# Performance work log

Hardware: AMD Instinct MI355X
Metric: run time of the kernel (lower is better)

Reference implementation:

```python
import jax, jax.numpy as jnp
import numpy as np
from jax import lax

R = 3                      # blob_r
S = 2 * R + 1              # 7: maxpool / neighborhood kernel size
THRESH = 0.997
PS_XY = 0.1                # vs_xy
PS_Z = 0.02                # vs_z
ZMIN = -2.0                # zrange[0]
K_PEAKS = 131072           # static upper bound replacing torch.nonzero

_offs = np.arange(S)
_gz, _gy, _gx = np.meshgrid(_offs, _offs, _offs, indexing='ij')  # patch axis order [z,y,x]
GZ = jnp.asarray(_gz.ravel(), dtype=jnp.int32)
GY = jnp.asarray(_gy.ravel(), dtype=jnp.int32)
GX = jnp.asarray(_gx.ravel(), dtype=jnp.int32)
# centroid filters: offsets -r..r along the matching patch axis (matches torch meshgrid layout)
FZ = jnp.asarray((_gz.ravel() - R).astype(np.float32))
FY = jnp.asarray((_gy.ravel() - R).astype(np.float32))
FX = jnp.asarray((_gx.ravel() - R).astype(np.float32))


def setup_inputs() -> dict:
    key = jax.random.key(0)
    pred_vol = jax.random.uniform(key, (1, 1, 128, 512, 512), dtype=jnp.float32)
    return {"pred_vol": pred_vol, "max_peaks": K_PEAKS}


def _forward(pred_vol, max_peaks):
    vol = pred_vol[0, 0]                               # [D,H,W]
    D, H, W = vol.shape
    thr = jnp.where(vol > THRESH, vol, 0.0)
    # MaxPool3d(kernel=2r+1, stride=1, padding=r) == SAME max window (pad with -inf)
    mp = lax.reduce_window(thr, -jnp.inf, lax.max, (S, S, S), (1, 1, 1), [(R, R)] * 3)
    conf = jnp.where((mp > 0.0) & (mp == thr), mp, 0.0)  # local maxima above threshold
    # fixed-size peak extraction (replaces torch.nonzero); zero-valued entries are padding
    vals, idx = lax.top_k(conf.reshape(-1), max_peaks)   # [K], [K]
    z = idx // (H * W)
    y = (idx % (H * W)) // W
    x = idx % W
    padv = jnp.pad(vol, R)                               # ConstantPad3d(r, 0)
    # gather (2r+1)^3 neighborhoods around each peak: [K, S^3]
    patches = padv[z[:, None] + GZ[None, :], y[:, None] + GY[None, :], x[:, None] + GX[None, :]]
    s0 = patches.sum(axis=1)                             # conv3d with ones filter == conf_rec sum
    xloc = jnp.einsum('kp,p->k', patches, FX) / s0
    yloc = jnp.einsum('kp,p->k', patches, FY) / s0
    zloc = jnp.einsum('kp,p->k', patches, FZ) / s0
    xf = x.astype(jnp.float32)
    yf = y.astype(jnp.float32)
    zf = z.astype(jnp.float32)
    xrec = (xf + xloc - (W - 1) / 2.0) * PS_XY
    yrec = (yf + yloc - (H - 1) / 2.0) * PS_XY
    zrec = (zf + zloc + 0.5) * PS_Z + ZMIN
    valid = vals > 0.0
    xyz = jnp.where(valid[:, None], jnp.stack((xrec, yrec, zrec), axis=1), 0.0)  # [K,3]
    out = jnp.concatenate([xyz, vals[:, None]], axis=1)  # [K,4] = (x,y,z,conf), padded rows are 0
    return out, valid


def reference(pred_vol, max_peaks):
    return _forward(pred_vol, max_peaks)
```

## Files before the change

kernel.cpp:

```cpp
#include <hip/hip_runtime.h>

#define DD 128
#define HH 512
#define WW 512
#define NVOX (DD*HH*WW)
#define THRESHV 0.997f
#define KPEAKS 131072
#define PEAK_CAP (1u<<18)
#define NBINS 65536


__global__ void k_init(unsigned* counters, unsigned* hist, unsigned long long* sorted) {
    unsigned t = blockIdx.x * 256u + threadIdx.x;
    if (t < 64) counters[t] = 0u;
    if (t < NBINS) hist[t] = 0u;
    if (t < PEAK_CAP) sorted[t] = 0ull;
}

__global__ void k_find(const float4* __restrict__ vol4, const float* __restrict__ vol,
                       unsigned* counters, unsigned* hist,
                       unsigned long long* keys, float4* psums) {
    __shared__ unsigned lcnt, pcnt, lbase;
    __shared__ unsigned cidx[512];
    __shared__ unsigned long long lbuf[256];
    __shared__ float4 sbuf[256];
    if (threadIdx.x == 0) { lcnt = 0; pcnt = 0; }
    __syncthreads();

    unsigned base4 = blockIdx.x * 2048u + threadIdx.x;
    float4 v[8];
#pragma unroll
    for (int i = 0; i < 8; i++) v[i] = vol4[base4 + i * 256u];
    unsigned m = 0u;
#pragma unroll
    for (int i = 0; i < 8; i++) {
        m |= (v[i].x > THRESHV ? 1u : 0u) << (4 * i);
        m |= (v[i].y > THRESHV ? 1u : 0u) << (4 * i + 1);
        m |= (v[i].z > THRESHV ? 1u : 0u) << (4 * i + 2);
        m |= (v[i].w > THRESHV ? 1u : 0u) << (4 * i + 3);
    }
    while (m) {
        int b = __ffs(m) - 1;
        m &= m - 1u;
        unsigned f4 = base4 + (unsigned)(b >> 2) * 256u;
        cidx[atomicAdd(&lcnt, 1u) & 511u] = f4 * 4u + (unsigned)(b & 3);
    }
    __syncthreads();

    unsigned n = lcnt > 512u ? 512u : lcnt;
    int lane = threadIdx.x & 63;
    int wv = threadIdx.x >> 6;
    int dz = lane / 7, dy = lane - dz * 7;
    for (unsigned ci = (unsigned)wv; ci < n; ci += 4u) {
        unsigned idx = cidx[ci];
        int z = idx >> 18, y = (idx >> 9) & 511, x = idx & 511;
        float center = vol[idx];
        int nz = z + dz - 3, ny = y + dy - 3;
        bool rowok = (lane < 49) && ((unsigned)nz < DD) && ((unsigned)ny < HH);
        size_t rowbase = rowok ? (((size_t)(unsigned)nz << 18) | ((size_t)(unsigned)ny << 9))
                               : (((size_t)z << 18) | ((size_t)y << 9));
        float rv[7];
        if (x >= 3 && x <= WW - 4) {
            float4 f0 = *(const float4*)(vol + rowbase + (unsigned)(x - 3));
            float4 f1 = *(const float4*)(vol + rowbase + (unsigned)(x + 1));
            rv[0] = f0.x; rv[1] = f0.y; rv[2] = f0.z; rv[3] = f0.w;
            rv[4] = f1.x; rv[5] = f1.y; rv[6] = f1.z;
        } else {
#pragma unroll
            for (int d = 0; d < 7; d++) {
                int nx = x + d - 3;
                bool ok = (unsigned)nx < WW;
                float vv = vol[rowbase + (unsigned)(ok ? nx : x)];
                rv[d] = ok ? vv : 0.f;
            }
        }
        if (!rowok) {
#pragma unroll
            for (int d = 0; d < 7; d++) rv[d] = 0.f;
        }
        bool kill = false;
        float s0r = 0.f, sxr = 0.f;
#pragma unroll
        for (int d = 0; d < 7; d++) {
            kill |= rv[d] > center;
            s0r += rv[d];
            sxr += rv[d] * (float)(d - 3);
        }
        if (!__any(kill)) {
            float s0 = s0r, sx = sxr;
            float sy = s0r * (float)(dy - 3);
            float sz = s0r * (float)(dz - 3);
            for (int off = 32; off; off >>= 1) {
                s0 += __shfl_down(s0, off);
                sx += __shfl_down(sx, off);
                sy += __shfl_down(sy, off);
                sz += __shfl_down(sz, off);
            }
            if (lane == 0) {
                unsigned bits = __float_as_uint(center);
                atomicAdd(&hist[(~bits) & 0xFFFFu], 1u);
                unsigned li = atomicAdd(&pcnt, 1u);
                if (li < 256u) {
                    lbuf[li] = ((unsigned long long)bits << 32) | idx;
                    sbuf[li] = make_float4(s0, sx, sy, sz);
                }
            }
        }
    }
    __syncthreads();
    if (threadIdx.x == 0) lbase = atomicAdd(&counters[1], pcnt);
    __syncthreads();
    unsigned np = pcnt > 256u ? 256u : pcnt;
    for (unsigned i = threadIdx.x; i < np; i += 256u) {
        unsigned p = lbase + i;
        if (p < PEAK_CAP) { keys[p] = lbuf[i]; psums[p] = sbuf[i]; }
    }
}

__global__ void k_scan(const unsigned* __restrict__ hist, unsigned* cursor) {
    __shared__ unsigned partial[1024];
    int t = threadIdx.x;
    const uint4* h4 = (const uint4*)(hist + t * 64);
    uint4 loc[16];
#pragma unroll
    for (int i = 0; i < 16; i++) loc[i] = h4[i];
    unsigned s = 0;
#pragma unroll
    for (int i = 0; i < 16; i++) s += loc[i].x + loc[i].y + loc[i].z + loc[i].w;
    partial[t] = s;
    __syncthreads();
    for (int off = 1; off < 1024; off <<= 1) {
        unsigned v = (t >= off) ? partial[t - off] : 0u;
        __syncthreads();
        partial[t] += v;
        __syncthreads();
    }
    unsigned run = (t == 0) ? 0u : partial[t - 1];
    uint4* c4 = (uint4*)(cursor + t * 64);
#pragma unroll
    for (int i = 0; i < 16; i++) {
        uint4 h = loc[i]; uint4 o;
        o.x = run; run += h.x;
        o.y = run; run += h.y;
        o.z = run; run += h.z;
        o.w = run; run += h.w;
        c4[i] = o;
    }
}

__global__ void k_scatter(const unsigned* __restrict__ counters,
                          const unsigned long long* __restrict__ keys,
                          unsigned* cursor, unsigned long long* sorted,
                          unsigned* sslot) {
    unsigned np = counters[1]; if (np > PEAK_CAP) np = PEAK_CAP;
    unsigned t = blockIdx.x * 256u + threadIdx.x;
    if (t < np) {
        unsigned long long key = keys[t];
        unsigned bits = (unsigned)(key >> 32);
        unsigned pos = atomicAdd(&cursor[(~bits) & 0xFFFFu], 1u);
        if (pos < PEAK_CAP) { sorted[pos] = key; sslot[pos] = t; }
    }
}

__global__ void k_tiefix(const unsigned long long* __restrict__ sorted,
                         const unsigned* __restrict__ sslot,
                         unsigned long long* outk, unsigned* oslot) {
    unsigned t = blockIdx.x * 256u + threadIdx.x;
    if (t >= PEAK_CAP) return;
    unsigned long long key = sorted[t];
    unsigned bits = (unsigned)(key >> 32);
    if (bits == 0u) { outk[t] = 0ull; return; }
    unsigned s = t;
    while (s > 0 && (unsigned)(sorted[s - 1] >> 32) == bits) s--;
    unsigned myidx = (unsigned)key;
    unsigned rank = 0, e = s;
    while (e < PEAK_CAP) {
        unsigned long long k2 = sorted[e];
        if ((unsigned)(k2 >> 32) != bits) break;
        if ((unsigned)k2 < myidx) rank++;
        e++;
    }
    outk[s + rank] = key;
    oslot[s + rank] = sslot[t];
}

__global__ void k_out(const unsigned long long* __restrict__ outk,
                      const unsigned* __restrict__ oslot,
                      const float4* __restrict__ psums,
                      float4* __restrict__ out, float* __restrict__ valid) {
    unsigned row = blockIdx.x * 256u + threadIdx.x;
    if (row >= KPEAKS) return;
    unsigned long long key = outk[row];
    unsigned bits = (unsigned)(key >> 32);
    if (bits == 0u) {
        out[row] = make_float4(0.f, 0.f, 0.f, 0.f);
        valid[row] = 0.f;
        return;
    }
    unsigned idx = (unsigned)key;
    int z = idx >> 18, y = (idx >> 9) & 511, x = idx & 511;
    float4 s = psums[oslot[row]];
    float val = __uint_as_float(bits);
    float xloc = s.y / s.x, yloc = s.z / s.x, zloc = s.w / s.x;
    float xr = ((float)x + xloc - (float)(WW - 1) * 0.5f) * 0.1f;
    float yr = ((float)y + yloc - (float)(HH - 1) * 0.5f) * 0.1f;
    float zr = ((float)z + zloc + 0.5f) * 0.02f - 2.0f;
    out[row] = make_float4(xr, yr, zr, val);
    valid[row] = 1.f;
}

extern "C" void kernel_launch(void* const* d_in, const int* in_sizes, int n_in,
                              void* d_out, int out_size, void* d_ws, size_t ws_size,
                              hipStream_t stream) {
    const float* vol = (const float*)d_in[0];

    char* w = (char*)d_ws;
    unsigned* counters = (unsigned*)w;
    unsigned* hist     = (unsigned*)(w + 1024);
    unsigned* cursor   = (unsigned*)(w + 1024 + NBINS * 4);
    char* w2 = w + 1024 + 2 * NBINS * 4;
    unsigned long long* keys   = (unsigned long long*)w2;
    unsigned long long* sorted = keys + PEAK_CAP;
    unsigned long long* keyout = sorted + PEAK_CAP;
    unsigned* sslot = (unsigned*)(keyout + PEAK_CAP);
    unsigned* oslot = sslot + PEAK_CAP;
    float4*   psums = (float4*)(oslot + PEAK_CAP);

    float* out_rows = (float*)d_out;
    float* valid = out_rows + (size_t)KPEAKS * 4;

    k_init<<<PEAK_CAP / 256, 256, 0, stream>>>(counters, hist, sorted);
    k_find<<<NVOX / 8192, 256, 0, stream>>>((const float4*)vol, vol, counters, hist, keys, psums);
    k_scan<<<1, 1024, 0, stream>>>(hist, cursor);
    k_scatter<<<PEAK_CAP / 256, 256, 0, stream>>>(counters, keys, cursor, sorted, sslot);
    k_tiefix<<<PEAK_CAP / 256, 256, 0, stream>>>(sorted, sslot, keyout, oslot);
    k_out<<<(KPEAKS + 255) / 256, 256, 0, stream>>>(keyout, oslot, psums, (float4*)out_rows, valid);
}
```

Baseline: 261.2 us.

## Process two candidates per wave and fuse tie-fix with output kernel

The candidate-verification loop now handles two candidate voxels per wavefront iteration, issuing both sets of neighborhood loads together, and takes the center value from a lane shuffle instead of a separate global load. The tie-fix kernel now writes final output rows directly, which removes the intermediate key/slot arrays and the separate output kernel. Zero-filling of padding rows moves into the scatter kernel for rows at or beyond the peak count. The aim is more memory-level parallelism in the find kernel and one fewer launch plus less intermediate traffic, at the cost of higher register use and wasted work when a candidate pair is unbalanced.

Result: no change. 261.7 us (+0.2%).

```diff
diff --git a/kernel.cpp b/kernel.cpp
--- a/kernel.cpp
+++ b/kernel.cpp
@@ -51,58 +51,112 @@
     int lane = threadIdx.x & 63;
     int wv = threadIdx.x >> 6;
     int dz = lane / 7, dy = lane - dz * 7;
-    for (unsigned ci = (unsigned)wv; ci < n; ci += 4u) {
-        unsigned idx = cidx[ci];
-        int z = idx >> 18, y = (idx >> 9) & 511, x = idx & 511;
-        float center = vol[idx];
-        int nz = z + dz - 3, ny = y + dy - 3;
-        bool rowok = (lane < 49) && ((unsigned)nz < DD) && ((unsigned)ny < HH);
-        size_t rowbase = rowok ? (((size_t)(unsigned)nz << 18) | ((size_t)(unsigned)ny << 9))
-                               : (((size_t)z << 18) | ((size_t)y << 9));
-        float rv[7];
-        if (x >= 3 && x <= WW - 4) {
-            float4 f0 = *(const float4*)(vol + rowbase + (unsigned)(x - 3));
-            float4 f1 = *(const float4*)(vol + rowbase + (unsigned)(x + 1));
-            rv[0] = f0.x; rv[1] = f0.y; rv[2] = f0.z; rv[3] = f0.w;
-            rv[4] = f1.x; rv[5] = f1.y; rv[6] = f1.z;
+    for (unsigned base = (unsigned)wv * 2u; base < n; base += 8u) {
+        bool has2 = (base + 1u < n);
+        unsigned idxA = cidx[base];
+        unsigned idxB = has2 ? cidx[base + 1u] : idxA;
+        int zA = idxA >> 18, yA = (idxA >> 9) & 511, xA = idxA & 511;
+        int zB = idxB >> 18, yB = (idxB >> 9) & 511, xB = idxB & 511;
+        int nzA = zA + dz - 3, nyA = yA + dy - 3;
+        int nzB = zB + dz - 3, nyB = yB + dy - 3;
+        bool rowokA = (lane < 49) && ((unsigned)nzA < DD) && ((unsigned)nyA < HH);
+        bool rowokB = (lane < 49) && ((unsigned)nzB < DD) && ((unsigned)nyB < HH);
+        size_t rbA = rowokA ? (((size_t)(unsigned)nzA << 18) | ((size_t)(unsigned)nyA << 9))
+                            : (((size_t)zA << 18) | ((size_t)yA << 9));
+        size_t rbB = rowokB ? (((size_t)(unsigned)nzB << 18) | ((size_t)(unsigned)nyB << 9))
+                            : (((size_t)zB << 18) | ((size_t)yB << 9));
+        float rvA[7], rvB[7];
+        bool intAB = (xA >= 3) && (xA <= WW - 4) && (xB >= 3) && (xB <= WW - 4);
+        if (intAB) {
+            float4 fA0 = *(const float4*)(vol + rbA + (unsigned)(xA - 3));
+            float4 fA1 = *(const float4*)(vol + rbA + (unsigned)(xA + 1));
+            float4 fB0 = *(const float4*)(vol + rbB + (unsigned)(xB - 3));
+            float4 fB1 = *(const float4*)(vol + rbB + (unsigned)(xB + 1));
+            rvA[0] = fA0.x; rvA[1] = fA0.y; rvA[2] = fA0.z; rvA[3] = fA0.w;
+            rvA[4] = fA1.x; rvA[5] = fA1.y; rvA[6] = fA1.z;
+            rvB[0] = fB0.x; rvB[1] = fB0.y; rvB[2] = fB0.z; rvB[3] = fB0.w;
+            rvB[4] = fB1.x; rvB[5] = fB1.y; rvB[6] = fB1.z;
         } else {
 #pragma unroll
             for (int d = 0; d < 7; d++) {
-                int nx = x + d - 3;
-                bool ok = (unsigned)nx < WW;
-                float vv = vol[rowbase + (unsigned)(ok ? nx : x)];
-                rv[d] = ok ? vv : 0.f;
-            }
-        }
-        if (!rowok) {
-#pragma unroll
-            for (int d = 0; d < 7; d++) rv[d] = 0.f;
-        }
-        bool kill = false;
-        float s0r = 0.f, sxr = 0.f;
-#pragma unroll
-        for (int d = 0; d < 7; d++) {
-            kill |= rv[d] > center;
-            s0r += rv[d];
-            sxr += rv[d] * (float)(d - 3);
-        }
-        if (!__any(kill)) {
-            float s0 = s0r, sx = sxr;
-            float sy = s0r * (float)(dy - 3);
-            float sz = s0r * (float)(dz - 3);
-            for (int off = 32; off; off >>= 1) {
-                s0 += __shfl_down(s0, off);
-                sx += __shfl_down(sx, off);
-                sy += __shfl_down(sy, off);
-                sz += __shfl_down(sz, off);
-            }
-            if (lane == 0) {
-                unsigned bits = __float_as_uint(center);
-                atomicAdd(&hist[(~bits) & 0xFFFFu], 1u);
-                unsigned li = atomicAdd(&pcnt, 1u);
-                if (li < 256u) {
-                    lbuf[li] = ((unsigned long long)bits << 32) | idx;
-                    sbuf[li] = make_float4(s0, sx, sy, sz);
+                int nxA = xA + d - 3;
+                bool okA = (unsigned)nxA < WW;
+                float va = vol[rbA + (unsigned)(okA ? nxA : xA)];
+                rvA[d] = okA ? va : 0.f;
+                int nxB = xB + d - 3;
+                bool okB = (unsigned)nxB < WW;
+                float vb = vol[rbB + (unsigned)(okB ? nxB : xB)];
+                rvB[d] = okB ? vb : 0.f;
+            }
+        }
+        if (!rowokA) {
+#pragma unroll
+            for (int d = 0; d < 7; d++) rvA[d] = 0.f;
+        }
+        if (!rowokB) {
+#pragma unroll
+            for (int d = 0; d < 7; d++) rvB[d] = 0.f;
+        }
+        float centerA = __shfl(rvA[3], 24);
+        float centerB = __shfl(rvB[3], 24);
+
+        {
+            bool kill = false;
+            float s0r = 0.f, sxr = 0.f;
+#pragma unroll
+            for (int d = 0; d < 7; d++) {
+                kill |= rvA[d] > centerA;
+                s0r += rvA[d];
+                sxr += rvA[d] * (float)(d - 3);
+            }
+            if (!__any(kill)) {
+                float s0 = s0r, sx = sxr;
+                float sy = s0r * (float)(dy - 3);
+                float sz = s0r * (float)(dz - 3);
+                for (int off = 32; off; off >>= 1) {
+                    s0 += __shfl_down(s0, off);
+                    sx += __shfl_down(sx, off);
+                    sy += __shfl_down(sy, off);
+                    sz += __shfl_down(sz, off);
+                }
+                if (lane == 0) {
+                    unsigned bits = __float_as_uint(centerA);
+                    atomicAdd(&hist[(~bits) & 0xFFFFu], 1u);
+                    unsigned li = atomicAdd(&pcnt, 1u);
+                    if (li < 256u) {
+                        lbuf[li] = ((unsigned long long)bits << 32) | idxA;
+                        sbuf[li] = make_float4(s0, sx, sy, sz);
+                    }
+                }
+            }
+        }
+        if (has2) {
+            bool kill = false;
+            float s0r = 0.f, sxr = 0.f;
+#pragma unroll
+            for (int d = 0; d < 7; d++) {
+                kill |= rvB[d] > centerB;
+                s0r += rvB[d];
+                sxr += rvB[d] * (float)(d - 3);
+            }
+            if (!__any(kill)) {
+                float s0 = s0r, sx = sxr;
+                float sy = s0r * (float)(dy - 3);
+                float sz = s0r * (float)(dz - 3);
+                for (int off = 32; off; off >>= 1) {
+                    s0 += __shfl_down(s0, off);
+                    sx += __shfl_down(sx, off);
+                    sy += __shfl_down(sy, off);
+                    sz += __shfl_down(sz, off);
+                }
+                if (lane == 0) {
+                    unsigned bits = __float_as_uint(centerB);
+                    atomicAdd(&hist[(~bits) & 0xFFFFu], 1u);
+                    unsigned li = atomicAdd(&pcnt, 1u);
+                    if (li < 256u) {
+                        lbuf[li] = ((unsigned long long)bits << 32) | idxB;
+                        sbuf[li] = make_float4(s0, sx, sy, sz);
+                    }
                 }
             }
         }
@@ -151,7 +205,8 @@
 __global__ void k_scatter(const unsigned* __restrict__ counters,
                           const unsigned long long* __restrict__ keys,
                           unsigned* cursor, unsigned long long* sorted,
-                          unsigned* sslot) {
+                          unsigned* sslot,
+                          float4* __restrict__ out, float* __restrict__ valid) {
     unsigned np = counters[1]; if (np > PEAK_CAP) np = PEAK_CAP;
     unsigned t = blockIdx.x * 256u + threadIdx.x;
     if (t < np) {
@@ -159,17 +214,21 @@
         unsigned bits = (unsigned)(key >> 32);
         unsigned pos = atomicAdd(&cursor[(~bits) & 0xFFFFu], 1u);
         if (pos < PEAK_CAP) { sorted[pos] = key; sslot[pos] = t; }
-    }
-}
-
-__global__ void k_tiefix(const unsigned long long* __restrict__ sorted,
+    } else if (t < KPEAKS) {
+        out[t] = make_float4(0.f, 0.f, 0.f, 0.f);
+        valid[t] = 0.f;
+    }
+}
+
+__global__ void k_finish(const unsigned long long* __restrict__ sorted,
                          const unsigned* __restrict__ sslot,
-                         unsigned long long* outk, unsigned* oslot) {
+                         const float4* __restrict__ psums,
+                         float4* __restrict__ out, float* __restrict__ valid) {
     unsigned t = blockIdx.x * 256u + threadIdx.x;
     if (t >= PEAK_CAP) return;
     unsigned long long key = sorted[t];
     unsigned bits = (unsigned)(key >> 32);
-    if (bits == 0u) { outk[t] = 0ull; return; }
+    if (bits == 0u) return;
     unsigned s = t;
     while (s > 0 && (unsigned)(sorted[s - 1] >> 32) == bits) s--;
     unsigned myidx = (unsigned)key;
@@ -180,28 +239,13 @@
         if ((unsigned)k2 < myidx) rank++;
         e++;
     }
-    outk[s + rank] = key;
-    oslot[s + rank] = sslot[t];
-}
-
-__global__ void k_out(const unsigned long long* __restrict__ outk,
-                      const unsigned* __restrict__ oslot,
-                      const float4* __restrict__ psums,
-                      float4* __restrict__ out, float* __restrict__ valid) {
-    unsigned row = blockIdx.x * 256u + threadIdx.x;
+    unsigned row = s + rank;
     if (row >= KPEAKS) return;
-    unsigned long long key = outk[row];
-    unsigned bits = (unsigned)(key >> 32);
-    if (bits == 0u) {
-        out[row] = make_float4(0.f, 0.f, 0.f, 0.f);
-        valid[row] = 0.f;
-        return;
-    }
-    unsigned idx = (unsigned)key;
+    unsigned idx = myidx;
     int z = idx >> 18, y = (idx >> 9) & 511, x = idx & 511;
-    float4 s = psums[oslot[row]];
+    float4 ps = psums[sslot[t]];
     float val = __uint_as_float(bits);
-    float xloc = s.y / s.x, yloc = s.z / s.x, zloc = s.w / s.x;
+    float xloc = ps.y / ps.x, yloc = ps.z / ps.x, zloc = ps.w / ps.x;
     float xr = ((float)x + xloc - (float)(WW - 1) * 0.5f) * 0.1f;
     float yr = ((float)y + yloc - (float)(HH - 1) * 0.5f) * 0.1f;
     float zr = ((float)z + zloc + 0.5f) * 0.02f - 2.0f;
@@ -221,10 +265,8 @@
     char* w2 = w + 1024 + 2 * NBINS * 4;
     unsigned long long* keys   = (unsigned long long*)w2;
     unsigned long long* sorted = keys + PEAK_CAP;
-    unsigned long long* keyout = sorted + PEAK_CAP;
-    unsigned* sslot = (unsigned*)(keyout + PEAK_CAP);
-    unsigned* oslot = sslot + PEAK_CAP;
-    float4*   psums = (float4*)(oslot + PEAK_CAP);
+    unsigned* sslot = (unsigned*)(sorted + PEAK_CAP);
+    float4*   psums = (float4*)(sslot + PEAK_CAP);
 
     float* out_rows = (float*)d_out;
     float* valid = out_rows + (size_t)KPEAKS * 4;
@@ -232,7 +274,8 @@
     k_init<<<PEAK_CAP / 256, 256, 0, stream>>>(counters, hist, sorted);
     k_find<<<NVOX / 8192, 256, 0, stream>>>((const float4*)vol, vol, counters, hist, keys, psums);
     k_scan<<<1, 1024, 0, stream>>>(hist, cursor);
-    k_scatter<<<PEAK_CAP / 256, 256, 0, stream>>>(counters, keys, cursor, sorted, sslot);
-    k_tiefix<<<PEAK_CAP / 256, 256, 0, stream>>>(sorted, sslot, keyout, oslot);
-    k_out<<<(KPEAKS + 255) / 256, 256, 0, stream>>>(keyout, oslot, psums, (float4*)out_rows, valid);
-}
+    k_scatter<<<PEAK_CAP / 256, 256, 0, stream>>>(counters, keys, cursor, sorted, sslot,
+                                                  (float4*)out_rows, valid);
+    k_finish<<<PEAK_CAP / 256, 256, 0, stream>>>(sorted, sslot, psums,
+                                                 (float4*)out_rows, valid);
+}
```

## Flatten candidate neighborhood checks into per-row tasks and fuse tiefix with output

Applied to the files above, without the earlier changes.

The local-maximum check in k_find now spreads candidate×row tasks (49 per candidate) across all threads, accumulating sums and kill flags in shared memory with atomics. This replaces the old scheme of one wavefront per candidate, which left 15 of 64 lanes idle and serialised candidates over 4 waves. The tie-fix and output kernels are merged into one, padding rows are zeroed inside the scatter kernel, and the sorted-array clear in init is dropped, so there is one fewer launch and less memory traffic. The trade-off is shared-memory float atomic contention and a larger LDS footprint.

Result: slower. 330.4 us (+26.5%).

```diff
diff --git a/kernel.cpp b/kernel.cpp
--- a/kernel.cpp
+++ b/kernel.cpp
@@ -10,11 +10,10 @@
 #define NBINS 65536
 
 
-__global__ void k_init(unsigned* counters, unsigned* hist, unsigned long long* sorted) {
+__global__ void k_init(unsigned* counters, unsigned* hist) {
     unsigned t = blockIdx.x * 256u + threadIdx.x;
     if (t < 64) counters[t] = 0u;
     if (t < NBINS) hist[t] = 0u;
-    if (t < PEAK_CAP) sorted[t] = 0ull;
 }
 
 __global__ void k_find(const float4* __restrict__ vol4, const float* __restrict__ vol,
@@ -22,8 +21,10 @@
                        unsigned long long* keys, float4* psums) {
     __shared__ unsigned lcnt, pcnt, lbase;
     __shared__ unsigned cidx[512];
-    __shared__ unsigned long long lbuf[256];
-    __shared__ float4 sbuf[256];
+    __shared__ float    cval[512];
+    __shared__ float4   accs[512];
+    __shared__ unsigned killf[512];
+    __shared__ unsigned lidx[512];
     if (threadIdx.x == 0) { lcnt = 0; pcnt = 0; }
     __syncthreads();
 
@@ -48,17 +49,25 @@
     __syncthreads();
 
     unsigned n = lcnt > 512u ? 512u : lcnt;
-    int lane = threadIdx.x & 63;
-    int wv = threadIdx.x >> 6;
-    int dz = lane / 7, dy = lane - dz * 7;
-    for (unsigned ci = (unsigned)wv; ci < n; ci += 4u) {
-        unsigned idx = cidx[ci];
+    for (unsigned i = threadIdx.x; i < n; i += 256u) {
+        cval[i] = vol[cidx[i]];
+        accs[i] = make_float4(0.f, 0.f, 0.f, 0.f);
+        killf[i] = 0u;
+    }
+    __syncthreads();
+
+    unsigned ntask = n * 49u;
+    for (unsigned t = threadIdx.x; t < ntask; t += 256u) {
+        unsigned c = t / 49u;
+        unsigned r = t - c * 49u;
+        int dz = (int)(r / 7u);
+        int dy = (int)(r - (unsigned)dz * 7u);
+        unsigned idx = cidx[c];
+        float center = cval[c];
         int z = idx >> 18, y = (idx >> 9) & 511, x = idx & 511;
-        float center = vol[idx];
         int nz = z + dz - 3, ny = y + dy - 3;
-        bool rowok = (lane < 49) && ((unsigned)nz < DD) && ((unsigned)ny < HH);
-        size_t rowbase = rowok ? (((size_t)(unsigned)nz << 18) | ((size_t)(unsigned)ny << 9))
-                               : (((size_t)z << 18) | ((size_t)y << 9));
+        if ((unsigned)nz >= DD || (unsigned)ny >= HH) continue;
+        size_t rowbase = ((size_t)(unsigned)nz << 18) | ((size_t)(unsigned)ny << 9);
         float rv[7];
         if (x >= 3 && x <= WW - 4) {
             float4 f0 = *(const float4*)(vol + rowbase + (unsigned)(x - 3));
@@ -74,10 +83,6 @@
                 rv[d] = ok ? vv : 0.f;
             }
         }
-        if (!rowok) {
-#pragma unroll
-            for (int d = 0; d < 7; d++) rv[d] = 0.f;
-        }
         bool kill = false;
         float s0r = 0.f, sxr = 0.f;
 #pragma unroll
@@ -86,34 +91,33 @@
             s0r += rv[d];
             sxr += rv[d] * (float)(d - 3);
         }
-        if (!__any(kill)) {
-            float s0 = s0r, sx = sxr;
-            float sy = s0r * (float)(dy - 3);
-            float sz = s0r * (float)(dz - 3);
-            for (int off = 32; off; off >>= 1) {
-                s0 += __shfl_down(s0, off);
-                sx += __shfl_down(sx, off);
-                sy += __shfl_down(sy, off);
-                sz += __shfl_down(sz, off);
-            }
-            if (lane == 0) {
-                unsigned bits = __float_as_uint(center);
-                atomicAdd(&hist[(~bits) & 0xFFFFu], 1u);
-                unsigned li = atomicAdd(&pcnt, 1u);
-                if (li < 256u) {
-                    lbuf[li] = ((unsigned long long)bits << 32) | idx;
-                    sbuf[li] = make_float4(s0, sx, sy, sz);
-                }
-            }
+        if (kill) killf[c] = 1u;
+        atomicAdd(&accs[c].x, s0r);
+        atomicAdd(&accs[c].y, sxr);
+        atomicAdd(&accs[c].z, s0r * (float)(dy - 3));
+        atomicAdd(&accs[c].w, s0r * (float)(dz - 3));
+    }
+    __syncthreads();
+
+    for (unsigned i = threadIdx.x; i < n; i += 256u) {
+        if (!killf[i]) {
+            unsigned bits = __float_as_uint(cval[i]);
+            atomicAdd(&hist[(~bits) & 0xFFFFu], 1u);
+            unsigned li = atomicAdd(&pcnt, 1u);
+            lidx[li & 511u] = i;
         }
     }
     __syncthreads();
     if (threadIdx.x == 0) lbase = atomicAdd(&counters[1], pcnt);
     __syncthreads();
-    unsigned np = pcnt > 256u ? 256u : pcnt;
-    for (unsigned i = threadIdx.x; i < np; i += 256u) {
+    unsigned npk = pcnt > 512u ? 512u : pcnt;
+    for (unsigned i = threadIdx.x; i < npk; i += 256u) {
         unsigned p = lbase + i;
-        if (p < PEAK_CAP) { keys[p] = lbuf[i]; psums[p] = sbuf[i]; }
+        if (p < PEAK_CAP) {
+            unsigned c = lidx[i];
+            keys[p] = ((unsigned long long)__float_as_uint(cval[c]) << 32) | cidx[c];
+            psums[p] = accs[c];
+        }
     }
 }
 
@@ -151,7 +155,8 @@
 __global__ void k_scatter(const unsigned* __restrict__ counters,
                           const unsigned long long* __restrict__ keys,
                           unsigned* cursor, unsigned long long* sorted,
-                          unsigned* sslot) {
+                          unsigned* sslot,
+                          float4* __restrict__ out, float* __restrict__ valid) {
     unsigned np = counters[1]; if (np > PEAK_CAP) np = PEAK_CAP;
     unsigned t = blockIdx.x * 256u + threadIdx.x;
     if (t < np) {
@@ -159,49 +164,39 @@
         unsigned bits = (unsigned)(key >> 32);
         unsigned pos = atomicAdd(&cursor[(~bits) & 0xFFFFu], 1u);
         if (pos < PEAK_CAP) { sorted[pos] = key; sslot[pos] = t; }
-    }
-}
-
-__global__ void k_tiefix(const unsigned long long* __restrict__ sorted,
+    } else if (t < KPEAKS) {
+        out[t] = make_float4(0.f, 0.f, 0.f, 0.f);
+        valid[t] = 0.f;
+    }
+}
+
+__global__ void k_finish(const unsigned* __restrict__ counters,
+                         const unsigned long long* __restrict__ sorted,
                          const unsigned* __restrict__ sslot,
-                         unsigned long long* outk, unsigned* oslot) {
+                         const float4* __restrict__ psums,
+                         float4* __restrict__ out, float* __restrict__ valid) {
+    unsigned np = counters[1]; if (np > PEAK_CAP) np = PEAK_CAP;
     unsigned t = blockIdx.x * 256u + threadIdx.x;
-    if (t >= PEAK_CAP) return;
+    if (t >= np) return;
     unsigned long long key = sorted[t];
     unsigned bits = (unsigned)(key >> 32);
-    if (bits == 0u) { outk[t] = 0ull; return; }
     unsigned s = t;
     while (s > 0 && (unsigned)(sorted[s - 1] >> 32) == bits) s--;
     unsigned myidx = (unsigned)key;
     unsigned rank = 0, e = s;
-    while (e < PEAK_CAP) {
+    while (e < np) {
         unsigned long long k2 = sorted[e];
         if ((unsigned)(k2 >> 32) != bits) break;
         if ((unsigned)k2 < myidx) rank++;
         e++;
     }
-    outk[s + rank] = key;
-    oslot[s + rank] = sslot[t];
-}
-
-__global__ void k_out(const unsigned long long* __restrict__ outk,
-                      const unsigned* __restrict__ oslot,
-                      const float4* __restrict__ psums,
-                      float4* __restrict__ out, float* __restrict__ valid) {
-    unsigned row = blockIdx.x * 256u + threadIdx.x;
+    unsigned row = s + rank;
     if (row >= KPEAKS) return;
-    unsigned long long key = outk[row];
-    unsigned bits = (unsigned)(key >> 32);
-    if (bits == 0u) {
-        out[row] = make_float4(0.f, 0.f, 0.f, 0.f);
-        valid[row] = 0.f;
-        return;
-    }
-    unsigned idx = (unsigned)key;
+    unsigned idx = myidx;
     int z = idx >> 18, y = (idx >> 9) & 511, x = idx & 511;
-    float4 s = psums[oslot[row]];
+    float4 ps = psums[sslot[t]];
     float val = __uint_as_float(bits);
-    float xloc = s.y / s.x, yloc = s.z / s.x, zloc = s.w / s.x;
+    float xloc = ps.y / ps.x, yloc = ps.z / ps.x, zloc = ps.w / ps.x;
     float xr = ((float)x + xloc - (float)(WW - 1) * 0.5f) * 0.1f;
     float yr = ((float)y + yloc - (float)(HH - 1) * 0.5f) * 0.1f;
     float zr = ((float)z + zloc + 0.5f) * 0.02f - 2.0f;
@@ -221,18 +216,17 @@
     char* w2 = w + 1024 + 2 * NBINS * 4;
     unsigned long long* keys   = (unsigned long long*)w2;
     unsigned long long* sorted = keys + PEAK_CAP;
-    unsigned long long* keyout = sorted + PEAK_CAP;
-    unsigned* sslot = (unsigned*)(keyout + PEAK_CAP);
-    unsigned* oslot = sslot + PEAK_CAP;
-    float4*   psums = (float4*)(oslot + PEAK_CAP);
+    unsigned* sslot = (unsigned*)(sorted + PEAK_CAP);
+    float4*   psums = (float4*)(sslot + PEAK_CAP);
 
     float* out_rows = (float*)d_out;
     float* valid = out_rows + (size_t)KPEAKS * 4;
 
-    k_init<<<PEAK_CAP / 256, 256, 0, stream>>>(counters, hist, sorted);
+    k_init<<<NBINS / 256, 256, 0, stream>>>(counters, hist);
     k_find<<<NVOX / 8192, 256, 0, stream>>>((const float4*)vol, vol, counters, hist, keys, psums);
     k_scan<<<1, 1024, 0, stream>>>(hist, cursor);
-    k_scatter<<<PEAK_CAP / 256, 256, 0, stream>>>(counters, keys, cursor, sorted, sslot);
-    k_tiefix<<<PEAK_CAP / 256, 256, 0, stream>>>(sorted, sslot, keyout, oslot);
-    k_out<<<(KPEAKS + 255) / 256, 256, 0, stream>>>(keyout, oslot, psums, (float4*)out_rows, valid);
-}
+    k_scatter<<<PEAK_CAP / 256, 256, 0, stream>>>(counters, keys, cursor, sorted, sslot,
+                                                  (float4*)out_rows, valid);
+    k_finish<<<PEAK_CAP / 256, 256, 0, stream>>>(counters, sorted, sslot, psums,
+                                                 (float4*)out_rows, valid);
+}
```
